# Kernel tuning notes

Hardware: AMD Instinct MI355X
Metric: run time of the kernel (lower is better)

## Reference

```python
import jax, jax.numpy as jnp
import numpy as np

D_MODEL = 1024
N_HEADS = 16
B, T = 2, 2048


def setup_inputs() -> dict:
    key = jax.random.key(0)
    ks = jax.random.split(key, 5)
    scale = 1.0 / np.sqrt(D_MODEL)
    return {
        "x": jax.random.normal(ks[0], (B, T, D_MODEL), dtype=jnp.float32),
        "W_q": jax.random.normal(ks[1], (D_MODEL, D_MODEL), dtype=jnp.float32) * scale,
        "W_k": jax.random.normal(ks[2], (D_MODEL, D_MODEL), dtype=jnp.float32) * scale,
        "W_v": jax.random.normal(ks[3], (D_MODEL, D_MODEL), dtype=jnp.float32) * scale,
        "W_o": jax.random.normal(ks[4], (D_MODEL, D_MODEL), dtype=jnp.float32) * scale,
    }


def reference(x, W_q, W_k, W_v, W_o):
    Bn, Tn, D = x.shape
    H = N_HEADS
    Dh = D // H
    # nn.Linear(x) = x @ W.T ; weights stored as [out, in]
    q = (x @ W_q.T).reshape(Bn, Tn, H, Dh).transpose(0, 2, 1, 3)  # [B,H,T,Dh]
    k = (x @ W_k.T).reshape(Bn, Tn, H, Dh).transpose(0, 2, 1, 3)
    v = (x @ W_v.T).reshape(Bn, Tn, H, Dh).transpose(0, 2, 1, 3)
    scores = jnp.einsum("bhqd,bhkd->bhqk", q, k) / np.sqrt(Dh).astype(np.float32)
    attn = jax.nn.softmax(scores, axis=-1)  # [B,H,T,T]
    out = jnp.einsum("bhqk,bhkd->bhqd", attn, v)  # [B,H,T,Dh]
    out = out.transpose(0, 2, 1, 3).reshape(Bn, Tn, D)
    return out @ W_o.T
```

## Files before the change

### kernel.cpp

```cpp
#include <hip/hip_runtime.h>
#include <stdint.h>
#include <stddef.h>


typedef __bf16  bf16x8  __attribute__((ext_vector_type(8)));
typedef __bf16  bf16x4  __attribute__((ext_vector_type(4)));
typedef float   floatx4 __attribute__((ext_vector_type(4)));
typedef short   short4v __attribute__((ext_vector_type(4)));

#define DEV static __device__ __forceinline__

DEV void ld_g2l16(const void* g, void* l) {
    __builtin_amdgcn_global_load_lds(
        (__attribute__((address_space(1))) void*)g,
        (__attribute__((address_space(3))) void*)l,
        16, 0, 0);
}

DEV floatx4 mfma16(bf16x4 a, bf16x4 b, floatx4 c) {
#if defined(__HIP_DEVICE_COMPILE__)
    return __builtin_amdgcn_mfma_f32_16x16x16bf16_1k(
        __builtin_bit_cast(short4v, a), __builtin_bit_cast(short4v, b),
        c, 0, 0, 0);
#else
    (void)a; (void)b;
    return c;
#endif
}

#define WK_SCALE 0.18033688011112042f

__global__ __launch_bounds__(256) void cvt_all(
    const float* __restrict__ x,
    const float* __restrict__ wq, const float* __restrict__ wk,
    const float* __restrict__ wv, const float* __restrict__ wo,
    __bf16* __restrict__ xb,
    __bf16* __restrict__ wqb, __bf16* __restrict__ wkb,
    __bf16* __restrict__ wvb, __bf16* __restrict__ wob)
{
    unsigned u = blockIdx.x * 256u + threadIdx.x;
    const float* src;
    __bf16* dst;
    unsigned off;
    float mul = 1.0f;
    if (u < 1048576u) {
        src = x; dst = xb; off = u;
    } else {
        unsigned u2 = u - 1048576u;
        unsigned sel = u2 >> 18;
        off = u2 & 0x3FFFFu;
        src = (sel == 0) ? wq : (sel == 1) ? wk : (sel == 2) ? wv : wo;
        dst = (sel == 0) ? wqb : (sel == 1) ? wkb : (sel == 2) ? wvb : wob;
        if (sel == 1) mul = WK_SCALE;
    }
    float4 f = *(const float4*)(src + (size_t)off * 4);
    bf16x4 o = { (__bf16)(f.x * mul), (__bf16)(f.y * mul),
                 (__bf16)(f.z * mul), (__bf16)(f.w * mul) };
    *(bf16x4*)(dst + (size_t)off * 4) = o;
}

template<int BM, int NMAT, bool OUT_F32>
__global__ __launch_bounds__(256) void gemm_bt(
    const __bf16* __restrict__ A,
    const __bf16* __restrict__ B0, const __bf16* __restrict__ B1,
    const __bf16* __restrict__ B2,
    void* __restrict__ C0, void* __restrict__ C1, void* __restrict__ C2)
{
    constexpr int Kd = 1024;
    constexpr int N  = 1024;
    constexpr int MI = BM / 32;
    constexpr int NA = BM / 64;
    __shared__ __bf16 As[BM * 32];
    __shared__ __bf16 Bs[128 * 32];

    const int t    = threadIdx.x;
    const int wid  = __builtin_amdgcn_readfirstlane(t >> 6);
    const int lane = t & 63;
    const int quad = lane >> 4;
    const int l15  = lane & 15;

    const int bx  = blockIdx.x;
    const int mat = (NMAT > 1) ? (bx >> 3) : 0;
    const int bn  = (NMAT > 1) ? (bx & 7)  : bx;
    const int bm  = blockIdx.y;
    const __bf16* Bm = (mat == 0) ? B0 : (mat == 1) ? B1 : B2;

    const __bf16* pA[NA];
    const __bf16* pB[2];
#pragma unroll
    for (int i = 0; i < NA; ++i) {
        int c    = i * 256 + t;
        int row  = c >> 2;
        int g    = (c & 3) ^ ((row >> 1) & 3);
        pA[i] = A + (size_t)(bm * BM + row) * Kd + g * 8;
    }
#pragma unroll
    for (int i = 0; i < 2; ++i) {
        int c    = i * 256 + t;
        int row  = c >> 2;
        int g    = (c & 3) ^ ((row >> 1) & 3);
        pB[i] = Bm + (size_t)(bn * 128 + row) * Kd + g * 8;
    }

    const int wm = wid >> 1;
    const int wn = wid & 1;
    const int slotr = quad ^ ((l15 >> 1) & 3);

    floatx4 acc[MI][4];
    const floatx4 z = { 0.f, 0.f, 0.f, 0.f };
#pragma unroll
    for (int i = 0; i < MI; ++i)
#pragma unroll
        for (int j = 0; j < 4; ++j) acc[i][j] = z;

    for (int kb = 0; kb < Kd; kb += 32) {
        __syncthreads();
#pragma unroll
        for (int i = 0; i < NA; ++i)
            ld_g2l16(pA[i] + kb, (char*)As + i * 4096 + wid * 1024);
#pragma unroll
        for (int i = 0; i < 2; ++i)
            ld_g2l16(pB[i] + kb, (char*)Bs + i * 4096 + wid * 1024);
        __syncthreads();

        bf16x8 af[MI], bf[4];
#pragma unroll
        for (int i = 0; i < MI; ++i) {
            int rowA = wm * (BM / 2) + i * 16 + l15;
            af[i] = *(const bf16x8*)&As[rowA * 32 + slotr * 8];
        }
#pragma unroll
        for (int j = 0; j < 4; ++j) {
            int rowB = wn * 64 + j * 16 + l15;
            bf[j] = *(const bf16x8*)&Bs[rowB * 32 + slotr * 8];
        }
#pragma unroll
        for (int i = 0; i < MI; ++i)
#pragma unroll
            for (int j = 0; j < 4; ++j)
                acc[i][j] = __builtin_amdgcn_mfma_f32_16x16x32_bf16(
                    af[i], bf[j], acc[i][j], 0, 0, 0);
    }

    void* Cv = (mat == 0) ? C0 : (mat == 1) ? C1 : C2;
    const int row0 = bm * BM + wm * (BM / 2);
    const int col0 = bn * 128 + wn * 64;
#pragma unroll
    for (int i = 0; i < MI; ++i)
#pragma unroll
        for (int j = 0; j < 4; ++j)
#pragma unroll
            for (int r = 0; r < 4; ++r) {
                int grow = row0 + i * 16 + quad * 4 + r;
                int gcol = col0 + j * 16 + l15;
                if (OUT_F32)
                    ((float*)Cv)[(size_t)grow * N + gcol] = acc[i][j][r];
                else
                    ((__bf16*)Cv)[(size_t)grow * N + gcol] = (__bf16)acc[i][j][r];
            }
}

__global__ __launch_bounds__(256) void transpose_v(
    const __bf16* __restrict__ V, __bf16* __restrict__ Vt)
{
    __shared__ __bf16 tile[64 * 72];
    const int t  = threadIdx.x;
    const int kt = blockIdx.x;
    const int bh = blockIdx.y;
    const int b  = bh >> 4, h = bh & 15;

#pragma unroll
    for (int rr = 0; rr < 64; rr += 32) {
        int row = rr + (t >> 3), ch = t & 7;
        uint4 v = *(const uint4*)(V + (size_t)(b * 2048 + kt * 64 + row) * 1024
                                    + h * 64 + ch * 8);
        *(uint4*)&tile[row * 72 + ch * 8] = v;
    }
    __syncthreads();
#pragma unroll
    for (int dd = 0; dd < 64; dd += 32) {
        int d = dd + (t >> 3), ch = t & 7;
        bf16x8 val;
#pragma unroll
        for (int j = 0; j < 8; ++j) val[j] = tile[(ch * 8 + j) * 72 + d];
        *(bf16x8*)(Vt + (size_t)(bh * 64 + d) * 2048 + kt * 64 + ch * 8) = val;
    }
}

__global__ __launch_bounds__(512, 4) void flash_kernel(
    const __bf16* __restrict__ Q, const __bf16* __restrict__ K,
    const __bf16* __restrict__ Vt, __bf16* __restrict__ O)
{
    __shared__ __bf16 Qs[128 * 64];
    __shared__ __bf16 Ks[2][2][64 * 64];
    __shared__ __bf16 Vs[2][2][64 * 64];

    const int t    = threadIdx.x;
    const int wid  = __builtin_amdgcn_readfirstlane(t >> 6);
    const int half = wid >> 2;
    const int wsub = wid & 3;
    const int lane = t & 63;
    const int quad = lane >> 4;
    const int l15  = lane & 15;
    const int qt   = blockIdx.x;
    const int bh   = blockIdx.y;
    const int b    = bh >> 4, h = bh & 15;

#pragma unroll
    for (int i = 0; i < 2; ++i) {
        int c = i * 512 + t;
        int row = c >> 3;
        int g   = (c & 7) ^ (row & 7);
        ld_g2l16(Q + (size_t)(b * 2048 + qt * 128 + row) * 1024 + h * 64 + g * 8,
                 (char*)Qs + i * 8192 + wid * 1024);
    }
#define ISSUE_KV(IT, BUF)                                                      \
    do {                                                                       \
        int row_ = t >> 3;                                                     \
        int g_   = (t & 7) ^ (row_ & 7);                                       \
        ld_g2l16(K + (size_t)(b * 2048 + (IT) * 64 + row_) * 1024              \
                     + h * 64 + g_ * 8,                                        \
                 (char*)Ks[0][BUF] + wid * 1024);                              \
        ld_g2l16(K + (size_t)(b * 2048 + (16 + (IT)) * 64 + row_) * 1024       \
                     + h * 64 + g_ * 8,                                        \
                 (char*)Ks[1][BUF] + wid * 1024);                              \
        ld_g2l16(Vt + (size_t)(bh * 64 + row_) * 2048 + (IT) * 64 + g_ * 8,    \
                 (char*)Vs[0][BUF] + wid * 1024);                              \
        ld_g2l16(Vt + (size_t)(bh * 64 + row_) * 2048 + (16 + (IT)) * 64       \
                     + g_ * 8,                                                 \
                 (char*)Vs[1][BUF] + wid * 1024);                              \
    } while (0)

    ISSUE_KV(0, 0);
    __syncthreads();

    bf16x8 qf[2][2];
#pragma unroll
    for (int nb = 0; nb < 2; ++nb)
#pragma unroll
        for (int ks = 0; ks < 2; ++ks) {
            int row  = wsub * 32 + nb * 16 + l15;
            int slot = (ks * 4 + quad) ^ (row & 7);
            qf[nb][ks] = *(const bf16x8*)&Qs[row * 64 + slot * 8];
        }

    int koff[2];
#pragma unroll
    for (int ks = 0; ks < 2; ++ks)
        koff[ks] = l15 * 128 + (((ks * 4 + quad) ^ (l15 & 7)) << 4);
    int voff[4];
#pragma unroll
    for (int k16 = 0; k16 < 4; ++k16)
        voff[k16] = l15 * 128 + (((k16 * 2 + (quad >> 1)) ^ (l15 & 7)) << 4)
                  + (quad & 1) * 8;

    const floatx4 z = { 0.f, 0.f, 0.f, 0.f };
    floatx4 o[2][4];
#pragma unroll
    for (int nb = 0; nb < 2; ++nb)
#pragma unroll
        for (int nd = 0; nd < 4; ++nd) o[nb][nd] = z;
    float lsum[2] = { 0.f, 0.f };

#pragma unroll 2
    for (int it = 0; it < 16; ++it) {
        const int cur = it & 1;
        if (it) __syncthreads();
        if (it < 15) ISSUE_KV(it + 1, cur ^ 1);

        const char* kbase = (const char*)Ks[half][cur];
        const char* vbase = (const char*)Vs[half][cur];
#pragma unroll
        for (int kt16 = 0; kt16 < 4; ++kt16) {
            floatx4 s[2] = { z, z };
#pragma unroll
            for (int ks = 0; ks < 2; ++ks) {
                bf16x8 kf = *(const bf16x8*)(kbase + kt16 * 2048 + koff[ks]);
#pragma unroll
                for (int nb = 0; nb < 2; ++nb)
                    s[nb] = __builtin_amdgcn_mfma_f32_16x16x32_bf16(
                        kf, qf[nb][ks], s[nb], 0, 0, 0);
            }
            bf16x4 pb[2];
#pragma unroll
            for (int nb = 0; nb < 2; ++nb) {
                float p0 = __builtin_amdgcn_exp2f(s[nb][0]);
                float p1 = __builtin_amdgcn_exp2f(s[nb][1]);
                float p2 = __builtin_amdgcn_exp2f(s[nb][2]);
                float p3 = __builtin_amdgcn_exp2f(s[nb][3]);
                lsum[nb] += (p0 + p1) + (p2 + p3);
                bf16x4 pw = { (__bf16)p0, (__bf16)p1, (__bf16)p2, (__bf16)p3 };
                pb[nb] = pw;
            }
#pragma unroll
            for (int nd = 0; nd < 4; ++nd) {
                bf16x4 va = *(const bf16x4*)(vbase + nd * 2048 + voff[kt16]);
#pragma unroll
                for (int nb = 0; nb < 2; ++nb)
                    o[nb][nd] = mfma16(va, pb[nb], o[nb][nd]);
            }
        }
    }
#undef ISSUE_KV

    __syncthreads();
    float* comb  = (float*)&Ks[0][0][0];
    float* lcomb = (float*)&Vs[0][0][0];
    if (half == 1) {
        float* my = comb + wsub * 2048;
#pragma unroll
        for (int nb = 0; nb < 2; ++nb)
#pragma unroll
            for (int nd = 0; nd < 4; ++nd)
                *(floatx4*)(my + (nb * 4 + nd) * 256 + lane * 4) = o[nb][nd];
        lcomb[wsub * 128 + lane]      = lsum[0];
        lcomb[wsub * 128 + 64 + lane] = lsum[1];
    }
    __syncthreads();
    if (half == 0) {
        float* pr = comb + wsub * 2048;
#pragma unroll
        for (int nb = 0; nb < 2; ++nb)
#pragma unroll
            for (int nd = 0; nd < 4; ++nd)
                o[nb][nd] += *(const floatx4*)(pr + (nb * 4 + nd) * 256 + lane * 4);
        lsum[0] += lcomb[wsub * 128 + lane];
        lsum[1] += lcomb[wsub * 128 + 64 + lane];

#pragma unroll
        for (int nb = 0; nb < 2; ++nb) {
            lsum[nb] += __shfl_xor(lsum[nb], 16);
            lsum[nb] += __shfl_xor(lsum[nb], 32);
        }
#pragma unroll
        for (int nb = 0; nb < 2; ++nb) {
            float inv = 1.f / lsum[nb];
            int token = qt * 128 + wsub * 32 + nb * 16 + l15;
#pragma unroll
            for (int nd = 0; nd < 4; ++nd) {
                bf16x4 ov = { (__bf16)(o[nb][nd][0] * inv),
                              (__bf16)(o[nb][nd][1] * inv),
                              (__bf16)(o[nb][nd][2] * inv),
                              (__bf16)(o[nb][nd][3] * inv) };
                *(bf16x4*)(O + (size_t)(b * 2048 + token) * 1024
                             + h * 64 + nd * 16 + quad * 4) = ov;
            }
        }
    }
}

extern "C" void kernel_launch(void* const* d_in, const int* in_sizes, int n_in,
                              void* d_out, int out_size, void* d_ws, size_t ws_size,
                              hipStream_t stream)
{
    const float* x  = (const float*)d_in[0];
    const float* wq = (const float*)d_in[1];
    const float* wk = (const float*)d_in[2];
    const float* wv = (const float*)d_in[3];
    const float* wo = (const float*)d_in[4];

    char* ws = (char*)d_ws;
    __bf16* xb  = (__bf16*)(ws + 0);
    __bf16* wqb = (__bf16*)(ws + 8388608);
    __bf16* wkb = (__bf16*)(ws + 10485760);
    __bf16* wvb = (__bf16*)(ws + 12582912);
    __bf16* wob = (__bf16*)(ws + 14680064);
    __bf16* Qb  = (__bf16*)(ws + 16777216);
    __bf16* Kb  = (__bf16*)(ws + 25165824);
    __bf16* Vb  = (__bf16*)(ws + 33554432);
    __bf16* Vtb = (__bf16*)(ws + 41943040);
    __bf16* Ob  = xb;

    cvt_all<<<8192, 256, 0, stream>>>(x, wq, wk, wv, wo, xb, wqb, wkb, wvb, wob);

    gemm_bt<128, 3, false><<<dim3(24, 32), 256, 0, stream>>>(
        xb, wqb, wkb, wvb, (void*)Qb, (void*)Kb, (void*)Vb);

    transpose_v<<<dim3(32, 32), 256, 0, stream>>>(Vb, Vtb);

    flash_kernel<<<dim3(16, 32), 512, 0, stream>>>(Qb, Kb, Vtb, Ob);

    gemm_bt<64, 1, true><<<dim3(8, 64), 256, 0, stream>>>(
        Ob, wob, nullptr, nullptr, d_out, nullptr, nullptr);
}
```

Measured before the change: 186.1 us.

## Fuse V transpose into QKV GEMM epilogue and shrink flash block to 4 waves

The QKV projection GEMM now writes V directly in transposed [B,H,Dh,T] layout from its epilogue, which removes the separate transpose kernel and one round trip of V through memory. The flash kernel moves from 8 waves to 4 waves per block, each wave handling 64 query rows instead of 32, and drops KV double buffering in favour of load-then-sync each iteration. Halving the LDS footprint and thread count aims to raise occupancy and reuse each K/V fragment across more query rows. The cost is that global-to-LDS loads no longer overlap with compute, and register pressure per wave rises.

```diff
diff --git a/kernel.cpp b/kernel.cpp
--- a/kernel.cpp
+++ b/kernel.cpp
@@ -59,7 +59,7 @@
     *(bf16x4*)(dst + (size_t)off * 4) = o;
 }
 
-template<int BM, int NMAT, bool OUT_F32>
+template<int BM, int NMAT, bool OUT_F32, bool TR_V>
 __global__ __launch_bounds__(256) void gemm_bt(
     const __bf16* __restrict__ A,
     const __bf16* __restrict__ B0, const __bf16* __restrict__ B1,
@@ -142,63 +142,55 @@
                     af[i], bf[j], acc[i][j], 0, 0, 0);
     }
 
-    void* Cv = (mat == 0) ? C0 : (mat == 1) ? C1 : C2;
     const int row0 = bm * BM + wm * (BM / 2);
     const int col0 = bn * 128 + wn * 64;
-#pragma unroll
-    for (int i = 0; i < MI; ++i)
-#pragma unroll
-        for (int j = 0; j < 4; ++j)
-#pragma unroll
-            for (int r = 0; r < 4; ++r) {
-                int grow = row0 + i * 16 + quad * 4 + r;
-                int gcol = col0 + j * 16 + l15;
-                if (OUT_F32)
-                    ((float*)Cv)[(size_t)grow * N + gcol] = acc[i][j][r];
-                else
-                    ((__bf16*)Cv)[(size_t)grow * N + gcol] = (__bf16)acc[i][j][r];
-            }
-}
-
-__global__ __launch_bounds__(256) void transpose_v(
-    const __bf16* __restrict__ V, __bf16* __restrict__ Vt)
-{
-    __shared__ __bf16 tile[64 * 72];
-    const int t  = threadIdx.x;
-    const int kt = blockIdx.x;
-    const int bh = blockIdx.y;
-    const int b  = bh >> 4, h = bh & 15;
-
-#pragma unroll
-    for (int rr = 0; rr < 64; rr += 32) {
-        int row = rr + (t >> 3), ch = t & 7;
-        uint4 v = *(const uint4*)(V + (size_t)(b * 2048 + kt * 64 + row) * 1024
-                                    + h * 64 + ch * 8);
-        *(uint4*)&tile[row * 72 + ch * 8] = v;
-    }
-    __syncthreads();
-#pragma unroll
-    for (int dd = 0; dd < 64; dd += 32) {
-        int d = dd + (t >> 3), ch = t & 7;
-        bf16x8 val;
-#pragma unroll
-        for (int j = 0; j < 8; ++j) val[j] = tile[(ch * 8 + j) * 72 + d];
-        *(bf16x8*)(Vt + (size_t)(bh * 64 + d) * 2048 + kt * 64 + ch * 8) = val;
-    }
-}
-
-__global__ __launch_bounds__(512, 4) void flash_kernel(
+
+    if (TR_V && mat == 2) {
+        __bf16* Vt = (__bf16*)C2;
+        const int bq    = bm >> 4;
+        const int tloc0 = (row0 & 2047) + quad * 4;
+#pragma unroll
+        for (int i = 0; i < MI; ++i)
+#pragma unroll
+            for (int j = 0; j < 4; ++j) {
+                int col = col0 + j * 16 + l15;
+                int hh  = col >> 6, dh = col & 63;
+                bf16x4 v = { (__bf16)acc[i][j][0], (__bf16)acc[i][j][1],
+                             (__bf16)acc[i][j][2], (__bf16)acc[i][j][3] };
+                *(bf16x4*)(Vt + ((size_t)(bq * 16 + hh) * 64 + dh) * 2048
+                              + tloc0 + i * 16) = v;
+            }
+    } else {
+        void* Cv = (mat == 0) ? C0 : (mat == 1) ? C1 : C2;
+#pragma unroll
+        for (int i = 0; i < MI; ++i)
+#pragma unroll
+            for (int j = 0; j < 4; ++j)
+#pragma unroll
+                for (int r = 0; r < 4; ++r) {
+                    int grow = row0 + i * 16 + quad * 4 + r;
+                    int gcol = col0 + j * 16 + l15;
+                    if (OUT_F32)
+                        ((float*)Cv)[(size_t)grow * N + gcol] = acc[i][j][r];
+                    else
+                        ((__bf16*)Cv)[(size_t)grow * N + gcol] =
+                            (__bf16)acc[i][j][r];
+                }
+    }
+}
+
+__global__ __launch_bounds__(256, 3) void flash_kernel(
     const __bf16* __restrict__ Q, const __bf16* __restrict__ K,
     const __bf16* __restrict__ Vt, __bf16* __restrict__ O)
 {
     __shared__ __bf16 Qs[128 * 64];
-    __shared__ __bf16 Ks[2][2][64 * 64];
-    __shared__ __bf16 Vs[2][2][64 * 64];
+    __shared__ __bf16 Ks[2][64 * 64];
+    __shared__ __bf16 Vs[2][64 * 64];
 
     const int t    = threadIdx.x;
     const int wid  = __builtin_amdgcn_readfirstlane(t >> 6);
-    const int half = wid >> 2;
-    const int wsub = wid & 3;
+    const int half = wid >> 1;
+    const int wsub = wid & 1;
     const int lane = t & 63;
     const int quad = lane >> 4;
     const int l15  = lane & 15;
@@ -207,39 +199,34 @@
     const int b    = bh >> 4, h = bh & 15;
 
 #pragma unroll
-    for (int i = 0; i < 2; ++i) {
-        int c = i * 512 + t;
+    for (int i = 0; i < 4; ++i) {
+        int c = i * 256 + t;
         int row = c >> 3;
         int g   = (c & 7) ^ (row & 7);
         ld_g2l16(Q + (size_t)(b * 2048 + qt * 128 + row) * 1024 + h * 64 + g * 8,
-                 (char*)Qs + i * 8192 + wid * 1024);
-    }
-#define ISSUE_KV(IT, BUF)                                                      \
-    do {                                                                       \
-        int row_ = t >> 3;                                                     \
-        int g_   = (t & 7) ^ (row_ & 7);                                       \
-        ld_g2l16(K + (size_t)(b * 2048 + (IT) * 64 + row_) * 1024              \
-                     + h * 64 + g_ * 8,                                        \
-                 (char*)Ks[0][BUF] + wid * 1024);                              \
-        ld_g2l16(K + (size_t)(b * 2048 + (16 + (IT)) * 64 + row_) * 1024       \
-                     + h * 64 + g_ * 8,                                        \
-                 (char*)Ks[1][BUF] + wid * 1024);                              \
-        ld_g2l16(Vt + (size_t)(bh * 64 + row_) * 2048 + (IT) * 64 + g_ * 8,    \
-                 (char*)Vs[0][BUF] + wid * 1024);                              \
-        ld_g2l16(Vt + (size_t)(bh * 64 + row_) * 2048 + (16 + (IT)) * 64       \
-                     + g_ * 8,                                                 \
-                 (char*)Vs[1][BUF] + wid * 1024);                              \
-    } while (0)
-
-    ISSUE_KV(0, 0);
+                 (char*)Qs + i * 4096 + wid * 1024);
+    }
+
+    const __bf16* pK[2];
+    const __bf16* pV[2];
+    int srow[2], sg[2];
+#pragma unroll
+    for (int i = 0; i < 2; ++i) {
+        int c = i * 256 + t;
+        srow[i] = c >> 3;
+        sg[i]   = (c & 7) ^ (srow[i] & 7);
+        pK[i] = K  + (size_t)(b * 2048 + srow[i]) * 1024 + h * 64 + sg[i] * 8;
+        pV[i] = Vt + (size_t)(bh * 64 + srow[i]) * 2048 + sg[i] * 8;
+    }
+
     __syncthreads();
 
-    bf16x8 qf[2][2];
-#pragma unroll
-    for (int nb = 0; nb < 2; ++nb)
+    bf16x8 qf[4][2];
+#pragma unroll
+    for (int nb = 0; nb < 4; ++nb)
 #pragma unroll
         for (int ks = 0; ks < 2; ++ks) {
-            int row  = wsub * 32 + nb * 16 + l15;
+            int row  = wsub * 64 + nb * 16 + l15;
             int slot = (ks * 4 + quad) ^ (row & 7);
             qf[nb][ks] = *(const bf16x8*)&Qs[row * 64 + slot * 8];
         }
@@ -255,35 +242,44 @@
                   + (quad & 1) * 8;
 
     const floatx4 z = { 0.f, 0.f, 0.f, 0.f };
-    floatx4 o[2][4];
-#pragma unroll
-    for (int nb = 0; nb < 2; ++nb)
+    floatx4 o[4][4];
+#pragma unroll
+    for (int nb = 0; nb < 4; ++nb)
 #pragma unroll
         for (int nd = 0; nd < 4; ++nd) o[nb][nd] = z;
-    float lsum[2] = { 0.f, 0.f };
-
-#pragma unroll 2
+    float lsum[4] = { 0.f, 0.f, 0.f, 0.f };
+
     for (int it = 0; it < 16; ++it) {
-        const int cur = it & 1;
-        if (it) __syncthreads();
-        if (it < 15) ISSUE_KV(it + 1, cur ^ 1);
-
-        const char* kbase = (const char*)Ks[half][cur];
-        const char* vbase = (const char*)Vs[half][cur];
+        __syncthreads();
+#pragma unroll
+        for (int i = 0; i < 2; ++i) {
+            ld_g2l16(pK[i] + (size_t)it * 65536,
+                     (char*)Ks[0] + i * 4096 + wid * 1024);
+            ld_g2l16(pK[i] + (size_t)(16 + it) * 65536,
+                     (char*)Ks[1] + i * 4096 + wid * 1024);
+            ld_g2l16(pV[i] + it * 64,
+                     (char*)Vs[0] + i * 4096 + wid * 1024);
+            ld_g2l16(pV[i] + (16 + it) * 64,
+                     (char*)Vs[1] + i * 4096 + wid * 1024);
+        }
+        __syncthreads();
+
+        const char* kbase = (const char*)Ks[half];
+        const char* vbase = (const char*)Vs[half];
 #pragma unroll
         for (int kt16 = 0; kt16 < 4; ++kt16) {
-            floatx4 s[2] = { z, z };
+            floatx4 s[4] = { z, z, z, z };
 #pragma unroll
             for (int ks = 0; ks < 2; ++ks) {
                 bf16x8 kf = *(const bf16x8*)(kbase + kt16 * 2048 + koff[ks]);
 #pragma unroll
-                for (int nb = 0; nb < 2; ++nb)
+                for (int nb = 0; nb < 4; ++nb)
                     s[nb] = __builtin_amdgcn_mfma_f32_16x16x32_bf16(
                         kf, qf[nb][ks], s[nb], 0, 0, 0);
             }
-            bf16x4 pb[2];
-#pragma unroll
-            for (int nb = 0; nb < 2; ++nb) {
+            bf16x4 pb[4];
+#pragma unroll
+            for (int nb = 0; nb < 4; ++nb) {
                 float p0 = __builtin_amdgcn_exp2f(s[nb][0]);
                 float p1 = __builtin_amdgcn_exp2f(s[nb][1]);
                 float p2 = __builtin_amdgcn_exp2f(s[nb][2]);
@@ -296,46 +292,42 @@
             for (int nd = 0; nd < 4; ++nd) {
                 bf16x4 va = *(const bf16x4*)(vbase + nd * 2048 + voff[kt16]);
 #pragma unroll
-                for (int nb = 0; nb < 2; ++nb)
+                for (int nb = 0; nb < 4; ++nb)
                     o[nb][nd] = mfma16(va, pb[nb], o[nb][nd]);
             }
         }
     }
-#undef ISSUE_KV
 
     __syncthreads();
-    float* comb  = (float*)&Ks[0][0][0];
-    float* lcomb = (float*)&Vs[0][0][0];
+    float* obuf = (wsub == 0) ? (float*)&Ks[0][0] : (float*)&Vs[0][0];
+    float* lbuf = (float*)&Qs[0] + wsub * 256;
     if (half == 1) {
-        float* my = comb + wsub * 2048;
-#pragma unroll
-        for (int nb = 0; nb < 2; ++nb)
+#pragma unroll
+        for (int nb = 0; nb < 4; ++nb)
 #pragma unroll
             for (int nd = 0; nd < 4; ++nd)
-                *(floatx4*)(my + (nb * 4 + nd) * 256 + lane * 4) = o[nb][nd];
-        lcomb[wsub * 128 + lane]      = lsum[0];
-        lcomb[wsub * 128 + 64 + lane] = lsum[1];
+                *(floatx4*)(obuf + (nb * 4 + nd) * 256 + lane * 4) = o[nb][nd];
+#pragma unroll
+        for (int nb = 0; nb < 4; ++nb) lbuf[nb * 64 + lane] = lsum[nb];
     }
     __syncthreads();
     if (half == 0) {
-        float* pr = comb + wsub * 2048;
-#pragma unroll
-        for (int nb = 0; nb < 2; ++nb)
+#pragma unroll
+        for (int nb = 0; nb < 4; ++nb)
 #pragma unroll
             for (int nd = 0; nd < 4; ++nd)
-                o[nb][nd] += *(const floatx4*)(pr + (nb * 4 + nd) * 256 + lane * 4);
-        lsum[0] += lcomb[wsub * 128 + lane];
-        lsum[1] += lcomb[wsub * 128 + 64 + lane];
-
-#pragma unroll
-        for (int nb = 0; nb < 2; ++nb) {
+                o[nb][nd] += *(const floatx4*)(obuf + (nb * 4 + nd) * 256
+                                               + lane * 4);
+#pragma unroll
+        for (int nb = 0; nb < 4; ++nb) {
+            lsum[nb] += lbuf[nb * 64 + lane];
             lsum[nb] += __shfl_xor(lsum[nb], 16);
             lsum[nb] += __shfl_xor(lsum[nb], 32);
         }
 #pragma unroll
-        for (int nb = 0; nb < 2; ++nb) {
+        for (int nb = 0; nb < 4; ++nb) {
             float inv = 1.f / lsum[nb];
-            int token = qt * 128 + wsub * 32 + nb * 16 + l15;
+            int token = qt * 128 + wsub * 64 + nb * 16 + l15;
 #pragma unroll
             for (int nd = 0; nd < 4; ++nd) {
                 bf16x4 ov = { (__bf16)(o[nb][nd][0] * inv),
@@ -367,19 +359,16 @@
     __bf16* wob = (__bf16*)(ws + 14680064);
     __bf16* Qb  = (__bf16*)(ws + 16777216);
     __bf16* Kb  = (__bf16*)(ws + 25165824);
-    __bf16* Vb  = (__bf16*)(ws + 33554432);
-    __bf16* Vtb = (__bf16*)(ws + 41943040);
+    __bf16* Vtb = (__bf16*)(ws + 33554432);
     __bf16* Ob  = xb;
 
     cvt_all<<<8192, 256, 0, stream>>>(x, wq, wk, wv, wo, xb, wqb, wkb, wvb, wob);
 
-    gemm_bt<128, 3, false><<<dim3(24, 32), 256, 0, stream>>>(
-        xb, wqb, wkb, wvb, (void*)Qb, (void*)Kb, (void*)Vb);
-
-    transpose_v<<<dim3(32, 32), 256, 0, stream>>>(Vb, Vtb);
-
-    flash_kernel<<<dim3(16, 32), 512, 0, stream>>>(Qb, Kb, Vtb, Ob);
-
-    gemm_bt<64, 1, true><<<dim3(8, 64), 256, 0, stream>>>(
+    gemm_bt<128, 3, false, true><<<dim3(24, 32), 256, 0, stream>>>(
+        xb, wqb, wkb, wvb, (void*)Qb, (void*)Kb, (void*)Vtb);
+
+    flash_kernel<<<dim3(16, 32), 256, 0, stream>>>(Qb, Kb, Vtb, Ob);
+
+    gemm_bt<64, 1, true, false><<<dim3(8, 64), 256, 0, stream>>>(
         Ob, wob, nullptr, nullptr, d_out, nullptr, nullptr);
 }
```

Result: slower. 293.1 us (+57.5%).
